# Performance work log

Hardware: AMD Instinct MI355X
Metric: run time of the kernel (lower is better)

Reference implementation:

```python
import jax, jax.numpy as jnp
import numpy as np

N_USER = 50000
N_ITEM = 100000
N = N_USER + N_ITEM
NNZ = 3_000_000
EMB = 64
BATCH = 4096


def _l2norm(x, eps=1e-12):
    # torch F.normalize(p=2, dim=1): x / max(||x||, eps)
    n = jnp.sqrt(jnp.sum(x * x, axis=1, keepdims=True))
    return x / jnp.maximum(n, eps)


def setup_inputs() -> dict:
    key = jax.random.key(0)
    ks = jax.random.split(key, 12)
    users = jax.random.randint(ks[0], (BATCH,), 0, N_USER, dtype=jnp.int64 if jax.config.jax_enable_x64 else jnp.int32)
    rows = jax.random.randint(ks[1], (NNZ,), 0, N, dtype=jnp.int32)
    cols = jax.random.randint(ks[2], (NNZ,), 0, N, dtype=jnp.int32)
    vals = jax.random.uniform(ks[3], (NNZ,), dtype=jnp.float32)
    user_emb = jax.random.normal(ks[4], (N_USER, EMB), dtype=jnp.float32) * 0.1
    item_emb = jax.random.normal(ks[5], (N_ITEM, EMB), dtype=jnp.float32) * 0.1
    W0 = jax.random.normal(ks[6], (EMB, EMB), dtype=jnp.float32) * 0.1
    b0 = jax.random.normal(ks[7], (1, EMB), dtype=jnp.float32) * 0.1
    W1 = jax.random.normal(ks[8], (EMB, EMB), dtype=jnp.float32) * 0.1
    b1 = jax.random.normal(ks[9], (1, EMB), dtype=jnp.float32) * 0.1
    W2 = jax.random.normal(ks[10], (EMB, EMB), dtype=jnp.float32) * 0.1
    b2 = jax.random.normal(ks[11], (1, EMB), dtype=jnp.float32) * 0.1
    return {"users": users, "rows": rows, "cols": cols, "vals": vals,
            "user_emb": user_emb, "item_emb": item_emb,
            "W0": W0, "b0": b0, "W1": W1, "b1": b1, "W2": W2, "b2": b2}


def reference(users, rows, cols, vals, user_emb, item_emb, W0, b0, W1, b1, W2, b2):
    ego = jnp.concatenate([user_emb, item_emb], axis=0)  # [N, EMB]
    total = ego  # all_embeddings[0]
    for W, b in ((W0, b0), (W1, b1), (W2, b2)):
        # SpMM: side[r] = sum_e vals[e] * ego[cols[e]] for rows[e]==r
        side = jax.ops.segment_sum(vals[:, None] * ego[cols], rows, num_segments=N)
        ego = jax.nn.leaky_relu(side @ W + b, negative_slope=0.2)
        total = total + _l2norm(ego)
    u_g = total[:N_USER]
    return u_g[users]  # [BATCH, EMB]
```

## Files before the change

kernel.cpp:

```cpp
#include <hip/hip_runtime.h>
#include <hip/hip_fp16.h>

#define N_USER 50000
#define N_ITEM 100000
#define NTOT   150000
#define NNZ    3000000
#define EMB    64
#define BATCH  4096

#define BROWS  128
#define NB     1172
#define BCAP   3008
#define CHUNK  6144
#define WIN    12288
#define EGO_BLKS 9375

typedef unsigned short u16;
typedef unsigned int   u32;
typedef unsigned long long u64;
typedef _Float16 f16;
typedef f16   f16x8 __attribute__((ext_vector_type(8)));
typedef float f32x4 __attribute__((ext_vector_type(4)));

__global__ __launch_bounds__(256) void k_init(const float4* __restrict__ ue4,
                                              const float4* __restrict__ ie4,
                                              uint2* __restrict__ ego,
                                              const float* __restrict__ ue,
                                              const int* __restrict__ users,
                                              float* __restrict__ out) {
    int bi = blockIdx.x, tid = threadIdx.x;
    if (bi < EGO_BLKS) {
        int i = bi * 256 + tid;
        const int UF4 = N_USER * EMB / 4;
        float4 f = (i < UF4) ? ue4[i] : ie4[i - UF4];
        __half2 h0 = __floats2half2_rn(f.x, f.y);
        __half2 h1 = __floats2half2_rn(f.z, f.w);
        ego[i] = make_uint2(*(u32*)&h0, *(u32*)&h1);
    } else {
        int t = (bi - EGO_BLKS) * 256 + tid;
        int w = t >> 6, lane = t & 63;
        int u = users[w];
        out[w * EMB + lane] = ue[(size_t)u * EMB + lane];
    }
}

__device__ __forceinline__ void scan_excl(const int* src, int* dst, int* wsum,
                                          int tid, int lane, int w) {
    int carry = 0;
    for (int base = 0; base < NB; base += 1024) {
        int i = base + tid;
        int x = (i < NB) ? src[i] : 0;
        int v = x;
#pragma unroll
        for (int off = 1; off < 64; off <<= 1) {
            int y = __shfl_up(v, off);
            if (lane >= off) v += y;
        }
        if (lane == 63) wsum[w] = v;
        __syncthreads();
        if (tid < 16) {
            int s = wsum[tid];
#pragma unroll
            for (int off = 1; off < 16; off <<= 1) {
                int y = __shfl_up(s, off);
                if (tid >= off) s += y;
            }
            wsum[tid] = s;
        }
        __syncthreads();
        int excl = carry + (w ? wsum[w - 1] : 0) + v - x;
        if (i < NB) dst[i] = excl;
        carry += wsum[15];
        __syncthreads();
    }
}

__global__ __launch_bounds__(1024) void k_bucket(const int* __restrict__ rows,
                                                 const int* __restrict__ cols,
                                                 const float* __restrict__ vals,
                                                 int* __restrict__ bcnt,
                                                 int2* __restrict__ bbuf) {
    __shared__ int2 stage[CHUNK];
    __shared__ u16  sbuck[CHUNK];
    __shared__ int histA[NB], histB[NB], cur[NB], gbase[NB];
    __shared__ int wsum[16];
    int tid = threadIdx.x, lane = tid & 63, w = tid >> 6;
    int start = blockIdx.x * WIN;
    int s2    = start + CHUNK;
    int n1 = min(start + CHUNK, NNZ) - start; n1 = n1 < 0 ? 0 : n1;
    int n2 = min(s2 + CHUNK, NNZ) - s2;       n2 = n2 < 0 ? 0 : n2;

    for (int i = tid; i < NB; i += 1024) { histA[i] = 0; histB[i] = 0; }
    __syncthreads();

    u32 ex[12], ev[12];
    int eb[12];
#pragma unroll
    for (int u = 0; u < 6; ++u) {
        int i = u * 1024 + tid;
        if (i < n1) {
            int e = start + i;
            int r = rows[e];
            ex[u] = (u32)cols[e] | ((u32)(r & 127) << 18);
            ev[u] = (u32)__float_as_int(vals[e]);
            eb[u] = r >> 7;
            atomicAdd(&histA[eb[u]], 1);
        }
    }
#pragma unroll
    for (int u = 0; u < 6; ++u) {
        int i = u * 1024 + tid;
        if (i < n2) {
            int e = s2 + i;
            int r = rows[e];
            ex[u + 6] = (u32)cols[e] | ((u32)(r & 127) << 18);
            ev[u + 6] = (u32)__float_as_int(vals[e]);
            eb[u + 6] = r >> 7;
            atomicAdd(&histB[eb[u + 6]], 1);
        }
    }
    __syncthreads();

    for (int i = tid; i < NB; i += 1024) {
        int t = histA[i] + histB[i];
        gbase[i] = t ? atomicAdd(&bcnt[i * 16], t) : 0;
    }
    scan_excl(histA, cur, wsum, tid, lane, w);

#pragma unroll
    for (int u = 0; u < 6; ++u) {
        int i = u * 1024 + tid;
        if (i < n1) {
            int pos = atomicAdd(&cur[eb[u]], 1);
            stage[pos] = make_int2((int)ex[u], (int)ev[u]);
            sbuck[pos] = (u16)eb[u];
        }
    }
    __syncthreads();
    for (int j = tid; j < n1; j += 1024) {
        int b = sbuck[j];
        int pos = gbase[b] + (j - (cur[b] - histA[b]));
        if (pos < BCAP)
            bbuf[(size_t)b * BCAP + pos] = stage[j];
    }
    __syncthreads();

    scan_excl(histB, cur, wsum, tid, lane, w);
#pragma unroll
    for (int u = 0; u < 6; ++u) {
        int i = u * 1024 + tid;
        if (i < n2) {
            int pos = atomicAdd(&cur[eb[u + 6]], 1);
            stage[pos] = make_int2((int)ex[u + 6], (int)ev[u + 6]);
            sbuck[pos] = (u16)eb[u + 6];
        }
    }
    __syncthreads();
    for (int j = tid; j < n2; j += 1024) {
        int b = sbuck[j];
        int pos = gbase[b] + histA[b] + (j - (cur[b] - histB[b]));
        if (pos < BCAP)
            bbuf[(size_t)b * BCAP + pos] = stage[j];
    }
}

__global__ __launch_bounds__(512) void k_fused(const int* __restrict__ bcnt,
                                               const int2* __restrict__ bbuf,
                                               const f16* __restrict__ ego_in,
                                               const float* __restrict__ W,
                                               const float* __restrict__ bias,
                                               u16* __restrict__ ego_out) {
    __shared__ __align__(16) char ubuf[BCAP * 8];
    __shared__ f16  Wl[64 * 72];
    __shared__ int  hist[128], cur[128], rowptr[129];
    __shared__ int  ws2[2];
    int2* stg = (int2*)ubuf;
    f16*  S16 = (f16*)ubuf;
    int tid = threadIdx.x, lane = tid & 63, w = tid >> 6;

    int b = blockIdx.x;
    int cnt = min(bcnt[b * 16], BCAP);
    const int2* src = bbuf + (size_t)b * BCAP;

    for (int i = tid; i < 4096; i += 512) {
        int k = i >> 6, n = i & 63;
        Wl[n * 72 + k] = (f16)W[i];
    }
    if (tid < 128) hist[tid] = 0;
    __syncthreads();

    u32 fx[6], fv[6];
#pragma unroll
    for (int u = 0; u < 6; ++u) {
        int i = u * 512 + tid;
        if (i < cnt) {
            int2 e = src[i];
            fx[u] = (u32)e.x;
            fv[u] = (u32)e.y;
            atomicAdd(&hist[(fx[u] >> 18) & 127], 1);
        }
    }
    __syncthreads();

    int sx = 0, sv = 0;
    if (tid < 128) {
        sx = hist[tid]; sv = sx;
#pragma unroll
        for (int off = 1; off < 64; off <<= 1) {
            int y = __shfl_up(sv, off);
            if (lane >= off) sv += y;
        }
        if (lane == 63) ws2[tid >> 6] = sv;
    }
    __syncthreads();
    if (tid < 128) {
        int excl = sv - sx + ((tid >= 64) ? ws2[0] : 0);
        rowptr[tid] = excl;
        cur[tid]    = excl;
    }
    if (tid == 0) rowptr[128] = cnt;
    __syncthreads();

#pragma unroll
    for (int u = 0; u < 6; ++u) {
        int i = u * 512 + tid;
        if (i < cnt) {
            int pos = atomicAdd(&cur[(fx[u] >> 18) & 127], 1);
            stg[pos] = make_int2((int)fx[u], (int)fv[u]);
        }
    }
    __syncthreads();

    const char* egob = (const char*)ego_in;
    int slot = lane >> 3, d8 = lane & 7;
    int rA = w * 16 + slot;
    int rB = rA + 8;
    int eA = rowptr[rA], kA = rowptr[rA + 1];
    int eB = rowptr[rB], kB = rowptr[rB + 1];
    float accA[8], accB[8];
#pragma unroll
    for (int j = 0; j < 8; ++j) { accA[j] = 0.f; accB[j] = 0.f; }
    while (__any((eA < kA) || (eB < kB))) {
        bool a0 = eA < kA, a1 = (eA + 1) < kA;
        bool b0 = eB < kB, b1 = (eB + 1) < kB;
        uint4 gA0, gA1, gB0, gB1;
        float vA0 = 0.f, vA1 = 0.f, vB0 = 0.f, vB1 = 0.f;
        if (a0) {
            int2 p = stg[eA];
            gA0 = *(const uint4*)(egob + ((size_t)(p.x & 0x3FFFF) << 7) + d8 * 16);
            vA0 = __int_as_float(p.y);
        }
        if (a1) {
            int2 p = stg[eA + 1];
            gA1 = *(const uint4*)(egob + ((size_t)(p.x & 0x3FFFF) << 7) + d8 * 16);
            vA1 = __int_as_float(p.y);
        }
        if (b0) {
            int2 p = stg[eB];
            gB0 = *(const uint4*)(egob + ((size_t)(p.x & 0x3FFFF) << 7) + d8 * 16);
            vB0 = __int_as_float(p.y);
        }
        if (b1) {
            int2 p = stg[eB + 1];
            gB1 = *(const uint4*)(egob + ((size_t)(p.x & 0x3FFFF) << 7) + d8 * 16);
            vB1 = __int_as_float(p.y);
        }
        if (a0) {
            float2 f0 = __half22float2(*(const __half2*)&gA0.x);
            float2 f1 = __half22float2(*(const __half2*)&gA0.y);
            float2 f2 = __half22float2(*(const __half2*)&gA0.z);
            float2 f3 = __half22float2(*(const __half2*)&gA0.w);
            accA[0] = fmaf(vA0, f0.x, accA[0]); accA[1] = fmaf(vA0, f0.y, accA[1]);
            accA[2] = fmaf(vA0, f1.x, accA[2]); accA[3] = fmaf(vA0, f1.y, accA[3]);
            accA[4] = fmaf(vA0, f2.x, accA[4]); accA[5] = fmaf(vA0, f2.y, accA[5]);
            accA[6] = fmaf(vA0, f3.x, accA[6]); accA[7] = fmaf(vA0, f3.y, accA[7]);
        }
        if (a1) {
            float2 f0 = __half22float2(*(const __half2*)&gA1.x);
            float2 f1 = __half22float2(*(const __half2*)&gA1.y);
            float2 f2 = __half22float2(*(const __half2*)&gA1.z);
            float2 f3 = __half22float2(*(const __half2*)&gA1.w);
            accA[0] = fmaf(vA1, f0.x, accA[0]); accA[1] = fmaf(vA1, f0.y, accA[1]);
            accA[2] = fmaf(vA1, f1.x, accA[2]); accA[3] = fmaf(vA1, f1.y, accA[3]);
            accA[4] = fmaf(vA1, f2.x, accA[4]); accA[5] = fmaf(vA1, f2.y, accA[5]);
            accA[6] = fmaf(vA1, f3.x, accA[6]); accA[7] = fmaf(vA1, f3.y, accA[7]);
        }
        if (b0) {
            float2 f0 = __half22float2(*(const __half2*)&gB0.x);
            float2 f1 = __half22float2(*(const __half2*)&gB0.y);
            float2 f2 = __half22float2(*(const __half2*)&gB0.z);
            float2 f3 = __half22float2(*(const __half2*)&gB0.w);
            accB[0] = fmaf(vB0, f0.x, accB[0]); accB[1] = fmaf(vB0, f0.y, accB[1]);
            accB[2] = fmaf(vB0, f1.x, accB[2]); accB[3] = fmaf(vB0, f1.y, accB[3]);
            accB[4] = fmaf(vB0, f2.x, accB[4]); accB[5] = fmaf(vB0, f2.y, accB[5]);
            accB[6] = fmaf(vB0, f3.x, accB[6]); accB[7] = fmaf(vB0, f3.y, accB[7]);
        }
        if (b1) {
            float2 f0 = __half22float2(*(const __half2*)&gB1.x);
            float2 f1 = __half22float2(*(const __half2*)&gB1.y);
            float2 f2 = __half22float2(*(const __half2*)&gB1.z);
            float2 f3 = __half22float2(*(const __half2*)&gB1.w);
            accB[0] = fmaf(vB1, f0.x, accB[0]); accB[1] = fmaf(vB1, f0.y, accB[1]);
            accB[2] = fmaf(vB1, f1.x, accB[2]); accB[3] = fmaf(vB1, f1.y, accB[3]);
            accB[4] = fmaf(vB1, f2.x, accB[4]); accB[5] = fmaf(vB1, f2.y, accB[5]);
            accB[6] = fmaf(vB1, f3.x, accB[6]); accB[7] = fmaf(vB1, f3.y, accB[7]);
        }
        eA += 2; eB += 2;
    }
    __syncthreads();
    {
        f16x8 hA, hB;
#pragma unroll
        for (int j = 0; j < 8; ++j) { hA[j] = (f16)accA[j]; hB[j] = (f16)accB[j]; }
        *(f16x8*)&S16[rA * 72 + d8 * 8] = hA;
        *(f16x8*)&S16[rB * 72 + d8 * 8] = hB;
    }
    __syncthreads();

    int m = lane & 15, quad = lane >> 4;
    int rowbase = b * BROWS;
    int m0 = w * 16;
    f32x4 C[4] = {{0.f,0.f,0.f,0.f},{0.f,0.f,0.f,0.f},{0.f,0.f,0.f,0.f},{0.f,0.f,0.f,0.f}};
#pragma unroll
    for (int kk = 0; kk < 2; ++kk) {
        f16x8 A = *(const f16x8*)&S16[(m0 + m) * 72 + kk * 32 + quad * 8];
#pragma unroll
        for (int nt = 0; nt < 4; ++nt) {
            f16x8 B = *(const f16x8*)&Wl[(nt * 16 + m) * 72 + kk * 32 + quad * 8];
            C[nt] = __builtin_amdgcn_mfma_f32_16x16x32_f16(A, B, C[nt], 0, 0, 0);
        }
    }
#pragma unroll
    for (int nt = 0; nt < 4; ++nt) {
        float bv = bias[nt * 16 + m];
#pragma unroll
        for (int r = 0; r < 4; ++r) {
            int orow = rowbase + m0 + quad * 4 + r;
            float o = C[nt][r] + bv;
            o = o > 0.f ? o : 0.2f * o;
            if (orow < NTOT) {
                __half hh = __float2half(o);
                ego_out[(size_t)orow * EMB + nt * 16 + m] = *(u16*)&hh;
            }
        }
    }
}

__global__ __launch_bounds__(256) void k_accum(const __half* __restrict__ ego,
                                               const int* __restrict__ users,
                                               float* __restrict__ out) {
    int t = blockIdx.x * 256 + threadIdx.x;
    int w = t >> 6, lane = t & 63;
    int u = users[w];
    float x = __half2float(ego[(size_t)u * EMB + lane]);
    float ss = x * x;
#pragma unroll
    for (int off = 32; off; off >>= 1) ss += __shfl_xor(ss, off);
    float n = sqrtf(ss);
    out[w * EMB + lane] += x / fmaxf(n, 1e-12f);
}

extern "C" void kernel_launch(void* const* d_in, const int* in_sizes, int n_in,
                              void* d_out, int out_size, void* d_ws, size_t ws_size,
                              hipStream_t stream) {
    const int*   users = (const int*)d_in[0];
    const int*   rows  = (const int*)d_in[1];
    const int*   cols  = (const int*)d_in[2];
    const float* vals  = (const float*)d_in[3];
    const float* ue    = (const float*)d_in[4];
    const float* ie    = (const float*)d_in[5];
    const float* Ws[3] = {(const float*)d_in[6], (const float*)d_in[8], (const float*)d_in[10]};
    const float* bs[3] = {(const float*)d_in[7], (const float*)d_in[9], (const float*)d_in[11]};
    float* out = (float*)d_out;

    char* p = (char*)d_ws;
    f16*  egoA  = (f16*)p;  p += (size_t)NTOT * EMB * 2;
    f16*  egoB  = (f16*)p;  p += (size_t)NTOT * EMB * 2;
    int2* bbuf  = (int2*)p; p += (size_t)NB * BCAP * 8;
    int*  bcnt  = (int*)p;  p += (size_t)NB * 16 * 4;

    hipMemsetAsync(bcnt, 0, (size_t)NB * 16 * 4, stream);
    k_init<<<EGO_BLKS + (BATCH * EMB) / 256, 256, 0, stream>>>(
        (const float4*)ue, (const float4*)ie, (uint2*)egoA, ue, users, out);

    k_bucket<<<(NNZ + WIN - 1) / WIN, 1024, 0, stream>>>(rows, cols, vals, bcnt, bbuf);

    const int grids[3] = {NB, NB, (N_USER + BROWS - 1) / BROWS};
    f16* bufs[2] = {egoA, egoB};
    for (int l = 0; l < 3; ++l) {
        const f16* src = bufs[l & 1];
        f16*       dst = bufs[(l + 1) & 1];
        k_fused<<<grids[l], 512, 0, stream>>>(bcnt, bbuf, src, Ws[l], bs[l], (u16*)dst);
        k_accum<<<(BATCH * EMB) / 256, 256, 0, stream>>>((const __half*)dst, users, out);
    }
}
```

Before: 322.0 us.

## Merge init and bucketing kernels into one launch with single-chunk bucket blocks

The separate ego-conversion/output-init kernel and the COO bucketing kernel are merged into one launch, with extra blocks doing the fp16 conversion and output seeding alongside the bucketing blocks. Each bucketing block now handles one 6144-edge chunk instead of two, which doubles the bucketing block count and removes the second scan and scatter pass per block. This is meant to cut a launch, let the two independent jobs overlap, and spread bucketing over more blocks. In exchange, the conversion blocks are padded to 1024 threads but still reserve the large shared-memory footprint, and more global atomics hit the per-bucket counters.

```diff
diff --git a/kernel.cpp b/kernel.cpp
--- a/kernel.cpp
+++ b/kernel.cpp
@@ -12,8 +12,10 @@
 #define NB     1172
 #define BCAP   3008
 #define CHUNK  6144
-#define WIN    12288
-#define EGO_BLKS 9375
+#define NBUCK  489
+#define EGO4   (NTOT * EMB / 4)
+#define EGOB   2344
+#define OUTB   ((BATCH * EMB) / 1024)
 
 typedef unsigned short u16;
 typedef unsigned int   u32;
@@ -21,28 +23,6 @@
 typedef _Float16 f16;
 typedef f16   f16x8 __attribute__((ext_vector_type(8)));
 typedef float f32x4 __attribute__((ext_vector_type(4)));
-
-__global__ __launch_bounds__(256) void k_init(const float4* __restrict__ ue4,
-                                              const float4* __restrict__ ie4,
-                                              uint2* __restrict__ ego,
-                                              const float* __restrict__ ue,
-                                              const int* __restrict__ users,
-                                              float* __restrict__ out) {
-    int bi = blockIdx.x, tid = threadIdx.x;
-    if (bi < EGO_BLKS) {
-        int i = bi * 256 + tid;
-        const int UF4 = N_USER * EMB / 4;
-        float4 f = (i < UF4) ? ue4[i] : ie4[i - UF4];
-        __half2 h0 = __floats2half2_rn(f.x, f.y);
-        __half2 h1 = __floats2half2_rn(f.z, f.w);
-        ego[i] = make_uint2(*(u32*)&h0, *(u32*)&h1);
-    } else {
-        int t = (bi - EGO_BLKS) * 256 + tid;
-        int w = t >> 6, lane = t & 63;
-        int u = users[w];
-        out[w * EMB + lane] = ue[(size_t)u * EMB + lane];
-    }
-}
 
 __device__ __forceinline__ void scan_excl(const int* src, int* dst, int* wsum,
                                           int tid, int lane, int w) {
@@ -75,90 +55,84 @@
     }
 }
 
-__global__ __launch_bounds__(1024) void k_bucket(const int* __restrict__ rows,
-                                                 const int* __restrict__ cols,
-                                                 const float* __restrict__ vals,
-                                                 int* __restrict__ bcnt,
-                                                 int2* __restrict__ bbuf) {
+__global__ __launch_bounds__(1024) void k_prep(const int* __restrict__ rows,
+                                               const int* __restrict__ cols,
+                                               const float* __restrict__ vals,
+                                               int* __restrict__ bcnt,
+                                               int2* __restrict__ bbuf,
+                                               const float4* __restrict__ ue4,
+                                               const float4* __restrict__ ie4,
+                                               uint2* __restrict__ ego,
+                                               const float* __restrict__ ue,
+                                               const int* __restrict__ users,
+                                               float* __restrict__ out) {
+    int bi = blockIdx.x, tid = threadIdx.x;
+    if (bi >= NBUCK) {
+        int bj = bi - NBUCK;
+        if (bj < EGOB) {
+            int i = bj * 1024 + tid;
+            if (i < EGO4) {
+                const int UF4 = N_USER * EMB / 4;
+                float4 f = (i < UF4) ? ue4[i] : ie4[i - UF4];
+                __half2 h0 = __floats2half2_rn(f.x, f.y);
+                __half2 h1 = __floats2half2_rn(f.z, f.w);
+                ego[i] = make_uint2(*(u32*)&h0, *(u32*)&h1);
+            }
+        } else {
+            int t = (bj - EGOB) * 1024 + tid;
+            int w = t >> 6, lane = t & 63;
+            int u = users[w];
+            out[w * EMB + lane] = ue[(size_t)u * EMB + lane];
+        }
+        return;
+    }
+
     __shared__ int2 stage[CHUNK];
     __shared__ u16  sbuck[CHUNK];
-    __shared__ int histA[NB], histB[NB], cur[NB], gbase[NB];
-    __shared__ int wsum[16];
-    int tid = threadIdx.x, lane = tid & 63, w = tid >> 6;
-    int start = blockIdx.x * WIN;
-    int s2    = start + CHUNK;
-    int n1 = min(start + CHUNK, NNZ) - start; n1 = n1 < 0 ? 0 : n1;
-    int n2 = min(s2 + CHUNK, NNZ) - s2;       n2 = n2 < 0 ? 0 : n2;
-
-    for (int i = tid; i < NB; i += 1024) { histA[i] = 0; histB[i] = 0; }
-    __syncthreads();
-
-    u32 ex[12], ev[12];
-    int eb[12];
+    __shared__ int  hist[NB], cur[NB], gbase[NB];
+    __shared__ int  wsum[16];
+    int lane = tid & 63, w = tid >> 6;
+    int start = bi * CHUNK;
+    int n = min(start + CHUNK, NNZ) - start;
+
+    for (int i = tid; i < NB; i += 1024) hist[i] = 0;
+    __syncthreads();
+
+    u32 ex[6], ev[6];
+    int eb[6];
 #pragma unroll
     for (int u = 0; u < 6; ++u) {
         int i = u * 1024 + tid;
-        if (i < n1) {
+        if (i < n) {
             int e = start + i;
             int r = rows[e];
             ex[u] = (u32)cols[e] | ((u32)(r & 127) << 18);
             ev[u] = (u32)__float_as_int(vals[e]);
             eb[u] = r >> 7;
-            atomicAdd(&histA[eb[u]], 1);
-        }
-    }
+            atomicAdd(&hist[eb[u]], 1);
+        }
+    }
+    __syncthreads();
+
+    for (int i = tid; i < NB; i += 1024) {
+        int h = hist[i];
+        gbase[i] = h ? atomicAdd(&bcnt[i * 16], h) : 0;
+    }
+    scan_excl(hist, cur, wsum, tid, lane, w);
+
 #pragma unroll
     for (int u = 0; u < 6; ++u) {
         int i = u * 1024 + tid;
-        if (i < n2) {
-            int e = s2 + i;
-            int r = rows[e];
-            ex[u + 6] = (u32)cols[e] | ((u32)(r & 127) << 18);
-            ev[u + 6] = (u32)__float_as_int(vals[e]);
-            eb[u + 6] = r >> 7;
-            atomicAdd(&histB[eb[u + 6]], 1);
-        }
-    }
-    __syncthreads();
-
-    for (int i = tid; i < NB; i += 1024) {
-        int t = histA[i] + histB[i];
-        gbase[i] = t ? atomicAdd(&bcnt[i * 16], t) : 0;
-    }
-    scan_excl(histA, cur, wsum, tid, lane, w);
-
-#pragma unroll
-    for (int u = 0; u < 6; ++u) {
-        int i = u * 1024 + tid;
-        if (i < n1) {
+        if (i < n) {
             int pos = atomicAdd(&cur[eb[u]], 1);
             stage[pos] = make_int2((int)ex[u], (int)ev[u]);
             sbuck[pos] = (u16)eb[u];
         }
     }
     __syncthreads();
-    for (int j = tid; j < n1; j += 1024) {
+    for (int j = tid; j < n; j += 1024) {
         int b = sbuck[j];
-        int pos = gbase[b] + (j - (cur[b] - histA[b]));
-        if (pos < BCAP)
-            bbuf[(size_t)b * BCAP + pos] = stage[j];
-    }
-    __syncthreads();
-
-    scan_excl(histB, cur, wsum, tid, lane, w);
-#pragma unroll
-    for (int u = 0; u < 6; ++u) {
-        int i = u * 1024 + tid;
-        if (i < n2) {
-            int pos = atomicAdd(&cur[eb[u + 6]], 1);
-            stage[pos] = make_int2((int)ex[u + 6], (int)ev[u + 6]);
-            sbuck[pos] = (u16)eb[u + 6];
-        }
-    }
-    __syncthreads();
-    for (int j = tid; j < n2; j += 1024) {
-        int b = sbuck[j];
-        int pos = gbase[b] + histA[b] + (j - (cur[b] - histB[b]));
+        int pos = gbase[b] + (j - (cur[b] - hist[b]));
         if (pos < BCAP)
             bbuf[(size_t)b * BCAP + pos] = stage[j];
     }
@@ -380,10 +354,9 @@
     int*  bcnt  = (int*)p;  p += (size_t)NB * 16 * 4;
 
     hipMemsetAsync(bcnt, 0, (size_t)NB * 16 * 4, stream);
-    k_init<<<EGO_BLKS + (BATCH * EMB) / 256, 256, 0, stream>>>(
+    k_prep<<<NBUCK + EGOB + OUTB, 1024, 0, stream>>>(
+        rows, cols, vals, bcnt, bbuf,
         (const float4*)ue, (const float4*)ie, (uint2*)egoA, ue, users, out);
-
-    k_bucket<<<(NNZ + WIN - 1) / WIN, 1024, 0, stream>>>(rows, cols, vals, bcnt, bbuf);
 
     const int grids[3] = {NB, NB, (N_USER + BROWS - 1) / BROWS};
     f16* bufs[2] = {egoA, egoB};
```

After: 322.5 us. No clear change (+0.1%).
